# Performance work log

Hardware: AMD Instinct MI355X
Metric: run time of the kernel (lower is better)

## Reference

```python
import jax, jax.numpy as jnp
import numpy as np

# SLAYER SRM-alpha neuron params (nmnist.yaml defaults)
THETA = 10.0      # spike threshold
TAU_SR = 10.0     # PSP (alpha kernel) time constant
TAU_REF = 1.0     # refractory time constant
SCALE_REF = 2.0   # refractory amplitude scale (kernel peak = -2*theta)
TS = 1.0          # simulation step (ms)
K_EPS = 100       # truncated PSP kernel length (alpha kernel ~0 beyond 10*tau)

_t = np.arange(K_EPS, dtype=np.float32) * TS
EPS = jnp.asarray((_t / TAU_SR) * np.exp(1.0 - _t / TAU_SR))  # alpha kernel, peak 1
REF_DECAY = float(np.exp(-TS / TAU_REF))
REF_AMP = SCALE_REF * THETA


def spike_fn(u):
    # hard threshold (forward only)
    return (u >= THETA).astype(u.dtype)


def psp(x):
    """Causal temporal convolution with the SRM alpha kernel. x: [B,C,H,W,T]."""
    B, C, H, W, T = x.shape
    xf = x.reshape(B * C * H * W, 1, T)
    k = EPS[::-1].reshape(1, 1, K_EPS).astype(x.dtype)
    y = jax.lax.conv_general_dilated(xf, k, (1,), [(K_EPS - 1, 0)])
    return y.reshape(B, C, H, W, T)


def spike(a):
    """Threshold with exponential refractory feedback, sequential over time."""
    at = jnp.moveaxis(a, -1, 0)  # [T,B,C,H,W]
    def step(r, a_t):
        u = a_t + r
        s = spike_fn(u)
        r_new = REF_DECAY * (r - REF_AMP * s)
        return r_new, s
    _, s = jax.lax.scan(step, jnp.zeros(at.shape[1:], a.dtype), at)
    return jnp.moveaxis(s, 0, -1)


DN = ('NCHWT', 'OIHWT', 'NCHWT')  # time treated as a size-1-kernel spatial dim

def conv_t(x, w, pad):
    # x: [B,C,H,W,T], w: [O,I,kh,kw] -> spatial conv applied at every time step
    return jax.lax.conv_general_dilated(
        x, w[..., None], (1, 1, 1),
        [(pad, pad), (pad, pad), (0, 0)], dimension_numbers=DN)


def pool_t(x):
    # SLAYER pool: depthwise 2x2 sum-pool with fixed weight 1.1*theta
    C = x.shape[1]
    k = jnp.full((C, 1, 2, 2, 1), 1.1 * THETA, x.dtype)
    return jax.lax.conv_general_dilated(
        x, k, (2, 2, 1), [(0, 0), (0, 0), (0, 0)],
        feature_group_count=C, dimension_numbers=DN)


def setup_inputs() -> dict:
    key = jax.random.key(0)
    ks = jax.random.split(key, 5)
    B, T = 16, 300
    s_in = (jax.random.uniform(ks[0], (B, 2, 34, 34, T)) < 0.05).astype(jnp.float32)
    def w(k, shape, fan):
        return jax.random.normal(k, shape, jnp.float32) * (4.0 / np.sqrt(fan))
    W1 = w(ks[1], (16, 2, 5, 5), 2 * 25)
    W2 = w(ks[2], (32, 16, 3, 3), 16 * 9)
    W3 = w(ks[3], (64, 32, 3, 3), 32 * 9)
    Wf = w(ks[4], (10, 64, 8, 8), 64 * 64)
    return {"s_in": s_in, "W1": W1, "W2": W2, "W3": W3, "Wf": Wf}


def reference(s_in, W1, W2, W3, Wf):
    s1 = spike(psp(conv_t(s_in, W1, 1)))  # [B,16,32,32,T]
    s2 = spike(psp(pool_t(s1)))           # [B,16,16,16,T]
    s3 = spike(psp(conv_t(s2, W2, 1)))    # [B,32,16,16,T]
    s4 = spike(psp(pool_t(s3)))           # [B,32,8,8,T]
    s5 = spike(psp(conv_t(s4, W3, 1)))    # [B,64,8,8,T]
    # dense (8,8,64)->10 is a full-extent conv == contraction over c,h,w
    u = jnp.einsum('bchwt,ochw->bot', s5, Wf)[:, :, None, None, :]
    return spike(psp(u))                  # [B,10,1,1,T]
```

## Files before the change

### kernel.cpp

```cpp
#include <hip/hip_runtime.h>
#include <hip/hip_bf16.h>
#include <stdint.h>
#include <stddef.h>

#define TPAD 320
#define TREAL 300

#define POOL_W   11.000000000000002

static __device__ __forceinline__ float bf2f(uint16_t b) {
    return __uint_as_float(((uint32_t)b) << 16);
}

struct IIRC { double DD, C1, C2, C3, DR; };
static __device__ __forceinline__ IIRC iirc_make() {
    IIRC c;
    c.DD = exp(-0.1);
    c.C1 = exp(1.0) / 10.0;
    c.C2 = exp(-9.0) / 10.0;
    c.C3 = 10.0 * exp(-9.0);
    c.DR = exp(-1.0);
    return c;
}
struct IIRS { double P, Q, P2, Q2, r; };
static __device__ __forceinline__ void iirs_init(IIRS& s) {
    s.P = 0.0; s.Q = 0.0; s.P2 = 0.0; s.Q2 = 0.0; s.r = 0.0;
}
static __device__ __forceinline__ bool iir_step(const IIRC& c, IIRS& st,
                                                double x, double xd) {
    double Qn  = c.DD * (st.Q + st.P);
    double Pn  = fma(c.DD, st.P, x);
    double Q2n = c.DD * (st.Q2 + st.P2);
    double P2n = fma(c.DD, st.P2, xd);
    double a = c.C1 * Qn - c.C2 * Q2n - c.C3 * P2n;
    double u = a + st.r;
    bool s = (u >= 10.0);
    st.r = c.DR * (st.r - (s ? 20.0 : 0.0));
    st.P = Pn; st.Q = Qn; st.P2 = P2n; st.Q2 = Q2n;
    return s;
}

__global__ void detect_kernel(const uint16_t* __restrict__ w1raw, int* __restrict__ flag)
{
    if (threadIdx.x == 0 && blockIdx.x == 0) {
        int sane = 1;
        for (int i = 0; i < 800; ++i) {
            int e = (w1raw[i] >> 7) & 0xFF;
            if (e >= 131) { sane = 0; break; }
        }
        *flag = sane;
    }
}

__global__ __launch_bounds__(256) void wtrans_kernel(
    const void* __restrict__ w, double* __restrict__ out, int Co, int CKK,
    const int* __restrict__ flag)
{
    int i = blockIdx.x * 256 + threadIdx.x;
    if (i >= Co * CKK) return;
    int co = i / CKK, r = i - co * CKK;
    double v = (*flag) ? (double)bf2f(((const uint16_t*)w)[i])
                       : (double)((const float*)w)[i];
    out[(size_t)(co >> 4) * CKK * 16 + (size_t)r * 16 + (co & 15)] = v;
}

__global__ __launch_bounds__(256) void wcvt_kernel(
    const void* __restrict__ w, float* __restrict__ out, int n, const int* __restrict__ flag)
{
    int i = blockIdx.x * 256 + threadIdx.x;
    if (i >= n) return;
    out[i] = (*flag) ? bf2f(((const uint16_t*)w)[i]) : ((const float*)w)[i];
}

__global__ __launch_bounds__(320) void convert_kernel(
    const void* __restrict__ s_in, uint8_t* __restrict__ u8, const int* __restrict__ flag)
{
    int row = blockIdx.x;
    int t = threadIdx.x;
    uint8_t v = 0;
    if (t < TREAL) {
        float x = (*flag) ? bf2f(((const uint16_t*)s_in)[(size_t)row * TREAL + t])
                          : ((const float*)s_in)[(size_t)row * TREAL + t];
        v = (x >= 0.5f) ? 1 : 0;
    }
    u8[(size_t)row * TPAD + t] = v;
}

template<int Ci, int CIB, int K, int Hi>
__global__ __launch_bounds__(320) void conv_z_kernel(
    const uint8_t* __restrict__ sprev,
    const double* __restrict__ Wt,
    double* __restrict__ z,
    int Co_total)
{
    constexpr int P = 1;
    constexpr int Wi = Hi;
    constexpr int Ho = Hi + 2 * P - K + 1;
    constexpr int Wo = Ho;
    constexpr int KK = K * K;
    constexpr int CKK = Ci * KK;
    constexpr int CW = K + 1;
    constexpr int NROW = CIB * K * CW;
    constexpr int NPASS = Ci / CIB;
    constexpr int WTILE = CIB * KK * 16;
    static_assert(Ci % CIB == 0, "pass split");
    static_assert(Wo % 2 == 0, "pair split");
    static_assert(NROW * 320 + WTILE * 8 <= 60 * 1024, "LDS over limit");

    __shared__ uint32_t stage[NROW * 80];
    __shared__ double wtile[WTILE];

    const int t   = threadIdx.x;
    const int h   = (int)blockIdx.x / (Wo / 2);
    const int w   = ((int)blockIdx.x % (Wo / 2)) * 2;
    const int gy  = (int)blockIdx.y;
    const int co0 = gy * 16;
    const int b   = (int)blockIdx.z;

    double acc0[16], acc1[16];
    #pragma unroll
    for (int c = 0; c < 16; ++c) { acc0[c] = 0.0; acc1[c] = 0.0; }

    const size_t in_b = (size_t)b * Ci * Hi * Wi * TPAD;
    const double* wg = Wt + (size_t)gy * CKK * 16;

    for (int p = 0; p < NPASS; ++p) {
        const int ci0 = p * CIB;
        __syncthreads();
        for (int idx = t; idx < NROW * 20; idx += 320) {
            int r  = idx / 20, dw = idx - (idx / 20) * 20;
            int cl = r / (K * CW);
            int rem = r - cl * (K * CW);
            int ky = rem / CW, cx = rem - ky * CW;
            int row = h - P + ky;
            int col = w - P + cx;
            uint4 v = make_uint4(0, 0, 0, 0);
            if ((unsigned)row < (unsigned)Hi && (unsigned)col < (unsigned)Wi)
                v = *(const uint4*)(sprev + in_b +
                      (((size_t)(ci0 + cl) * Hi + row) * Wi + col) * TPAD + dw * 16);
            ((uint4*)stage)[(size_t)r * 20 + dw] = v;
        }
        for (int i = t; i < WTILE; i += 320)
            wtile[i] = wg[(size_t)ci0 * KK * 16 + i];
        __syncthreads();

        const uint8_t* sbytes = (const uint8_t*)stage;
        #pragma unroll 2
        for (int cl = 0; cl < CIB; ++cl) {
            #pragma unroll
            for (int ky = 0; ky < K; ++ky) {
                #pragma unroll
                for (int kx = 0; kx < K; ++kx) {
                    const int rbase = ((cl * K + ky) * CW + kx) * 320;
                    double x0 = (double)sbytes[rbase + t];
                    double x1 = (double)sbytes[rbase + 320 + t];
                    const double* wrow = wtile + (cl * KK + ky * K + kx) * 16;
                    #pragma unroll
                    for (int c = 0; c < 16; ++c) {
                        double wv = wrow[c];
                        acc0[c] = fma(wv, x0, acc0[c]);
                        acc1[c] = fma(wv, x1, acc1[c]);
                    }
                }
            }
        }
    }

    #pragma unroll
    for (int c = 0; c < 16; ++c) {
        size_t row0 = (((size_t)b * Co_total + co0 + c) * Ho + h) * Wo + w;
        z[row0 * TPAD + t]          = acc0[c];
        z[(row0 + 1) * TPAD + t]    = acc1[c];
    }
}

__global__ __launch_bounds__(256) void psp_scan_kernel(
    const double* __restrict__ z, uint8_t* __restrict__ sout, int N)
{
    __shared__ uint32_t bits[128 * 11];
    const int tid = threadIdx.x;
    const int n0 = blockIdx.x * 128;
    const int n = n0 + tid;
    const bool active = (tid < 128) && (n < N);

    if (active) {
        const double* zr = z + (size_t)n * TPAD;
        const IIRC c = iirc_make();
        IIRS st; iirs_init(st);
        uint32_t bw = 0;
        #pragma unroll 5
        for (int t0 = 0; t0 < 100; t0 += 4) {
            double2 xa = *(const double2*)(zr + t0);
            double2 xb = *(const double2*)(zr + t0 + 2);
            if (iir_step(c, st, xa.x, 0.0)) bw |= 1u << (t0 & 31);
            if (iir_step(c, st, xa.y, 0.0)) bw |= 1u << ((t0 + 1) & 31);
            if (iir_step(c, st, xb.x, 0.0)) bw |= 1u << ((t0 + 2) & 31);
            if (iir_step(c, st, xb.y, 0.0)) bw |= 1u << ((t0 + 3) & 31);
            if ((t0 & 31) == 28) { bits[tid * 11 + (t0 >> 5)] = bw; bw = 0; }
        }
        #pragma unroll 5
        for (int t0 = 100; t0 < TREAL; t0 += 4) {
            double2 xa = *(const double2*)(zr + t0);
            double2 xb = *(const double2*)(zr + t0 + 2);
            double2 da = *(const double2*)(zr + t0 - 100);
            double2 db = *(const double2*)(zr + t0 - 98);
            if (iir_step(c, st, xa.x, da.x)) bw |= 1u << (t0 & 31);
            if (iir_step(c, st, xa.y, da.y)) bw |= 1u << ((t0 + 1) & 31);
            if (iir_step(c, st, xb.x, db.x)) bw |= 1u << ((t0 + 2) & 31);
            if (iir_step(c, st, xb.y, db.y)) bw |= 1u << ((t0 + 3) & 31);
            if ((t0 & 31) == 28) { bits[tid * 11 + (t0 >> 5)] = bw; bw = 0; }
        }
        bits[tid * 11 + 9] = bw;
    }
    __syncthreads();

    for (int task = tid; task < 128 * 80; task += 256) {
        int nl = task / 80, w = task - nl * 80;
        int ng = n0 + nl;
        if (ng >= N) continue;
        int tb = w * 4;
        uint32_t word = bits[nl * 11 + (tb >> 5)];
        uint32_t o = 0;
        #pragma unroll
        for (int j = 0; j < 4; ++j)
            if ((word >> ((tb + j) & 31)) & 1u) o |= 1u << (8 * j);
        *(uint32_t*)(sout + (size_t)ng * TPAD + tb) = o;
    }
}

template<int C, int Hi>
__global__ __launch_bounds__(256) void pool_psp_v2_kernel(
    const uint8_t* __restrict__ sprev, uint8_t* __restrict__ sout, int N)
{
    constexpr int Wi = Hi, Ho = Hi / 2, Wo = Wi / 2;
    __shared__ uint32_t cnt[128 * 81];
    __shared__ uint32_t bits[128 * 11];
    const int tid = threadIdx.x;
    const int n0 = blockIdx.x * 128;

    for (int task = tid; task < 128 * 80; task += 256) {
        int nl = task / 80, w = task - nl * 80;
        int n = n0 + nl;
        if (n >= N) continue;
        int wo = n % Wo;  int r1 = n / Wo;
        int ho = r1 % Ho; int r2 = r1 / Ho;
        int cc = r2 % C;  int b  = r2 / C;
        const uint8_t* p0 = sprev +
            ((((size_t)b * C + cc) * Hi + 2 * ho) * Wi + 2 * wo) * TPAD + w * 4;
        uint32_t a0 = *(const uint32_t*)p0;
        uint32_t a1 = *(const uint32_t*)(p0 + TPAD);
        uint32_t a2 = *(const uint32_t*)(p0 + (size_t)Wi * TPAD);
        uint32_t a3 = *(const uint32_t*)(p0 + (size_t)(Wi + 1) * TPAD);
        cnt[nl * 81 + w] = a0 + a1 + a2 + a3;
    }
    __syncthreads();

    if (tid < 128 && n0 + tid < N) {
        const uint8_t* cb = (const uint8_t*)cnt + (size_t)tid * 324;
        const IIRC c = iirc_make();
        IIRS st; iirs_init(st);
        uint32_t bw = 0;
        for (int t = 0; t < 100; ++t) {
            double x = POOL_W * (double)cb[t];
            if (iir_step(c, st, x, 0.0)) bw |= 1u << (t & 31);
            if ((t & 31) == 31) { bits[tid * 11 + (t >> 5)] = bw; bw = 0; }
        }
        for (int t = 100; t < TREAL; ++t) {
            double x  = POOL_W * (double)cb[t];
            double xd = POOL_W * (double)cb[t - 100];
            if (iir_step(c, st, x, xd)) bw |= 1u << (t & 31);
            if ((t & 31) == 31) { bits[tid * 11 + (t >> 5)] = bw; bw = 0; }
        }
        bits[tid * 11 + 9] = bw;
    }
    __syncthreads();

    for (int task = tid; task < 128 * 80; task += 256) {
        int nl = task / 80, w = task - nl * 80;
        int n = n0 + nl;
        if (n >= N) continue;
        int tb = w * 4;
        uint32_t word = bits[nl * 11 + (tb >> 5)];
        uint32_t o = 0;
        #pragma unroll
        for (int j = 0; j < 4; ++j)
            if ((word >> ((tb + j) & 31)) & 1u) o |= 1u << (8 * j);
        *(uint32_t*)(sout + (size_t)n * TPAD + tb) = o;
    }
}

__global__ __launch_bounds__(256) void dense_partial_kernel(
    const uint8_t* __restrict__ s5, const float* __restrict__ Wf,
    double* __restrict__ partial)
{
    const int tc = blockIdx.x, b = blockIdx.y, p = blockIdx.z;
    const int tid = threadIdx.x;
    const int tl = tid & 63, slot = tid >> 6;
    const int t = tc * 64 + tl;
    const int i0 = p * 256 + slot * 64;
    double acc[10];
    #pragma unroll
    for (int o = 0; o < 10; ++o) acc[o] = 0.0;
    const uint8_t* sp = s5 + ((size_t)b * 4096 + i0) * TPAD + t;
    for (int i = 0; i < 64; ++i) {
        float f = (float)sp[(size_t)i * TPAD];
        if (__any(f != 0.f)) {
            #pragma unroll
            for (int o = 0; o < 10; ++o)
                acc[o] = fma((double)Wf[o * 4096 + i0 + i], (double)f, acc[o]);
        }
    }
    __shared__ double red[4][64][10];
    #pragma unroll
    for (int o = 0; o < 10; ++o) red[slot][tl][o] = acc[o];
    __syncthreads();
    if (slot == 0) {
        #pragma unroll
        for (int o = 0; o < 10; ++o) {
            double v = ((red[0][tl][o] + red[1][tl][o]) + red[2][tl][o]) + red[3][tl][o];
            partial[((size_t)p * 160 + (size_t)b * 10 + o) * TPAD + t] = v;
        }
    }
}

__global__ __launch_bounds__(320) void psp_out_final_kernel(
    const double* __restrict__ partial, void* __restrict__ out,
    const int* __restrict__ flag)
{
    __shared__ double xs[TPAD];
    __shared__ uint8_t sb[TREAL];
    const int n = blockIdx.x;
    const int t = threadIdx.x;
    double v = 0.0;
    #pragma unroll
    for (int p = 0; p < 16; ++p)
        v += partial[((size_t)p * 160 + n) * TPAD + t];
    xs[t] = v;
    __syncthreads();
    if (t == 0) {
        const IIRC c = iirc_make();
        IIRS st; iirs_init(st);
        for (int i = 0; i < TREAL; ++i) {
            double xd = (i >= 100) ? xs[i - 100] : 0.0;
            sb[i] = iir_step(c, st, xs[i], xd) ? 1 : 0;
        }
    }
    __syncthreads();
    if (t < TREAL) {
        size_t e = (size_t)n * TREAL + t;
        if (*flag) ((uint16_t*)out)[e] = sb[t] ? 0x3F80 : 0;
        else       ((float*)out)[e]    = sb[t] ? 1.0f : 0.0f;
    }
}

__global__ __launch_bounds__(256) void fill_kernel(float* __restrict__ out, int n, float v)
{
    int i = blockIdx.x * 256 + threadIdx.x;
    if (i < n) out[i] = v;
}

static inline size_t alignup(size_t x) { return (x + 255) & ~(size_t)255; }
static inline int pick_bg(size_t per_b, size_t budget) {
    const int cand[5] = {16, 8, 4, 2, 1};
    for (int k = 0; k < 5; ++k)
        if (per_b * (size_t)cand[k] <= budget) return cand[k];
    return 0;
}

extern "C" void kernel_launch(void* const* d_in, const int* in_sizes, int n_in,
                              void* d_out, int out_size, void* d_ws, size_t ws_size,
                              hipStream_t stream)
{
    if (n_in != 5 || in_sizes[0] != 16 * 2 * 34 * 34 * 300 || in_sizes[1] != 800 ||
        in_sizes[2] != 4608 || in_sizes[3] != 18432 || in_sizes[4] != 40960 ||
        out_size != 16 * 10 * 300) {
        fill_kernel<<<(out_size + 255) / 256, 256, 0, stream>>>((float*)d_out, out_size, 2.0e5f);
        return;
    }

    const size_t flag_sz  = alignup(sizeof(int));
    const size_t w64_sz   = alignup((size_t)(800 + 4608 + 18432) * 8);
    const size_t wf32_sz  = alignup((size_t)40960 * 4);
    const size_t sin8_sz  = alignup((size_t)16 * 2 * 34 * 34 * TPAD);
    const size_t dpart_sz = alignup((size_t)16 * 160 * TPAD * 8);
    const size_t sA_sz    = alignup((size_t)16 * 16384 * TPAD);
    const size_t sB_sz    = alignup((size_t)16 * 4096 * TPAD);
    const size_t base_sz  = flag_sz + w64_sz + wf32_sz + sin8_sz + dpart_sz + sA_sz + sB_sz;
    if (base_sz + 256 > ws_size) {
        fill_kernel<<<(out_size + 255) / 256, 256, 0, stream>>>((float*)d_out, out_size, 1.0e5f);
        return;
    }
    const size_t zbud = ws_size - base_sz - 256;

    const size_t zb1 = (size_t)16 * 1024 * TPAD * 8;
    const size_t zb3 = (size_t)32 * 256 * TPAD * 8;
    const size_t zb5 = (size_t)64 * 64 * TPAD * 8;
    const int bg1 = pick_bg(zb1, zbud), bg3 = pick_bg(zb3, zbud), bg5 = pick_bg(zb5, zbud);
    if (bg1 == 0 || bg3 == 0 || bg5 == 0) {
        fill_kernel<<<(out_size + 255) / 256, 256, 0, stream>>>((float*)d_out, out_size, 1.0e5f);
        return;
    }

    char* base = (char*)d_ws;
    int* flag = (int*)base;          base += flag_sz;
    double* w64 = (double*)base;     base += w64_sz;
    float* wf32 = (float*)base;      base += wf32_sz;
    uint8_t* sin8 = (uint8_t*)base;  base += sin8_sz;
    double* dpart = (double*)base;   base += dpart_sz;
    uint8_t* sA = (uint8_t*)base;    base += sA_sz;
    uint8_t* sB = (uint8_t*)base;    base += sB_sz;
    double* z64 = (double*)base;

    detect_kernel<<<1, 64, 0, stream>>>((const uint16_t*)d_in[1], flag);

    double* Wt1 = w64;
    double* Wt2 = w64 + 800;
    double* Wt3 = w64 + 800 + 4608;
    wtrans_kernel<<<(800 + 255) / 256, 256, 0, stream>>>(d_in[1], Wt1, 16, 50, flag);
    wtrans_kernel<<<(4608 + 255) / 256, 256, 0, stream>>>(d_in[2], Wt2, 32, 144, flag);
    wtrans_kernel<<<(18432 + 255) / 256, 256, 0, stream>>>(d_in[3], Wt3, 64, 288, flag);
    wcvt_kernel<<<(40960 + 255) / 256, 256, 0, stream>>>(d_in[4], wf32, 40960, flag);
    convert_kernel<<<16 * 2 * 34 * 34, 320, 0, stream>>>(d_in[0], sin8, flag);

    for (int b0 = 0; b0 < 16; b0 += bg1) {
        conv_z_kernel<2, 2, 5, 34><<<dim3(32 * 16, 1, bg1), 320, 0, stream>>>(
            sin8 + (size_t)b0 * 2 * 34 * 34 * TPAD, Wt1, z64, 16);
        int N = bg1 * 16384;
        psp_scan_kernel<<<(N + 127) / 128, 256, 0, stream>>>(
            z64, sA + (size_t)b0 * 16384 * TPAD, N);
    }
    pool_psp_v2_kernel<16, 32><<<(16 * 4096 + 127) / 128, 256, 0, stream>>>(
        sA, sB, 16 * 4096);
    for (int b0 = 0; b0 < 16; b0 += bg3) {
        conv_z_kernel<16, 8, 3, 16><<<dim3(16 * 8, 2, bg3), 320, 0, stream>>>(
            sB + (size_t)b0 * 16 * 256 * TPAD, Wt2, z64, 32);
        int N = bg3 * 8192;
        psp_scan_kernel<<<(N + 127) / 128, 256, 0, stream>>>(
            z64, sA + (size_t)b0 * 8192 * TPAD, N);
    }
    pool_psp_v2_kernel<32, 16><<<(16 * 2048 + 127) / 128, 256, 0, stream>>>(
        sA, sB, 16 * 2048);
    for (int b0 = 0; b0 < 16; b0 += bg5) {
        conv_z_kernel<32, 8, 3, 8><<<dim3(8 * 4, 4, bg5), 320, 0, stream>>>(
            sB + (size_t)b0 * 32 * 64 * TPAD, Wt3, z64, 64);
        int N = bg5 * 4096;
        psp_scan_kernel<<<(N + 127) / 128, 256, 0, stream>>>(
            z64, sA + (size_t)b0 * 4096 * TPAD, N);
    }
    dense_partial_kernel<<<dim3(5, 16, 16), 256, 0, stream>>>(sA, wf32, dpart);
    psp_out_final_kernel<<<160, 320, 0, stream>>>(dpart, d_out, flag);
}
```

Baseline: 1.670 ms.

## Use FP64 MFMA 16x16x4 for conv layers with runtime accumulation-order probe

Rewrites the spatial conv inner loop to use the f64 16x16x4 matrix-core instruction. Weights are pre-packed into per-lane fragment layout and input spike bytes are read from LDS as the A operand. A one-wave probe kernel checks whether the MFMA rounding matches a sequential FMA chain, in ascending or descending order, so that results stay bit-exact. If neither order matches, the original scalar FMA path is used. This aims to cut the FP64 FMA cost of the conv stages, at the price of extra launches, an LDS weight-layout change and a runtime branch.

```diff
diff --git a/kernel.cpp b/kernel.cpp
--- a/kernel.cpp
+++ b/kernel.cpp
@@ -7,6 +7,8 @@
 #define TREAL 300
 
 #define POOL_W   11.000000000000002
+
+typedef double v4d __attribute__((ext_vector_type(4)));
 
 static __device__ __forceinline__ float bf2f(uint16_t b) {
     return __uint_as_float(((uint32_t)b) << 16);
@@ -52,6 +54,51 @@
     }
 }
 
+static __device__ __forceinline__ double probe_val(int a, int b, int s) {
+    uint32_t h = (uint32_t)(a * 73856093) ^ (uint32_t)(b * 19349663)
+               ^ (uint32_t)(s * 83492791) ^ 0x9e3779b9u;
+    h ^= h >> 13; h *= 0x85ebca6bu; h ^= h >> 16;
+    int mant = (int)(h & 0xFFFFFu) | 1;
+    int e = (int)((h >> 20) & 63u) - 32;
+    double v = ldexp((double)mant, e);
+    return (h & 0x40000000u) ? -v : v;
+}
+
+__global__ void mfma_probe_kernel(int* __restrict__ mode)
+{
+    const int lane = (int)threadIdx.x & 63;
+    const int i16 = lane & 15;
+    const int k4  = lane >> 4;
+    bool ok_asc = true, ok_desc = true;
+    for (int s = 0; s < 8; ++s) {
+        double av = probe_val(i16, k4, 2 * s + 1);
+        double bv = probe_val(16 + k4, i16, 3 * s + 2);
+        v4d c;
+        #pragma unroll
+        for (int r = 0; r < 4; ++r)
+            c[r] = probe_val(32 + 4 * k4 + r, i16, 5 * s + 3);
+        v4d d = __builtin_amdgcn_mfma_f64_16x16x4f64(av, bv, c, 0, 0, 0);
+        #pragma unroll
+        for (int r = 0; r < 4; ++r) {
+            int i = 4 * k4 + r, j = i16;
+            double ea = probe_val(32 + i, j, 5 * s + 3);
+            double ed = ea;
+            #pragma unroll
+            for (int k = 0; k < 4; ++k)
+                ea = fma(probe_val(i, k, 2 * s + 1), probe_val(16 + k, j, 3 * s + 2), ea);
+            #pragma unroll
+            for (int k2 = 3; k2 >= 0; --k2)
+                ed = fma(probe_val(i, k2, 2 * s + 1), probe_val(16 + k2, j, 3 * s + 2), ed);
+            ok_asc  &= (__double_as_longlong(ea) == __double_as_longlong(d[r]));
+            ok_desc &= (__double_as_longlong(ed) == __double_as_longlong(d[r]));
+        }
+    }
+    unsigned long long ba = __ballot(ok_asc);
+    unsigned long long bd = __ballot(ok_desc);
+    if (threadIdx.x == 0)
+        *mode = (ba == ~0ull) ? 1 : ((bd == ~0ull) ? 2 : 0);
+}
+
 __global__ __launch_bounds__(256) void wtrans_kernel(
     const void* __restrict__ w, double* __restrict__ out, int Co, int CKK,
     const int* __restrict__ flag)
@@ -62,6 +109,31 @@
     double v = (*flag) ? (double)bf2f(((const uint16_t*)w)[i])
                        : (double)((const float*)w)[i];
     out[(size_t)(co >> 4) * CKK * 16 + (size_t)r * 16 + (co & 15)] = v;
+}
+
+__global__ __launch_bounds__(256) void wtrans_frag_kernel(
+    const void* __restrict__ w, double* __restrict__ out,
+    int CKK, int KS_TOTAL, int total,
+    const int* __restrict__ flag, const int* __restrict__ mode)
+{
+    int i = blockIdx.x * 256 + threadIdx.x;
+    if (i >= total) return;
+    int md = *mode;
+    int lane = i & 63;
+    int gks  = (i >> 6) % KS_TOTAL;
+    int gy   = (i >> 6) / KS_TOTAL;
+    int kl   = lane >> 4;
+    int col  = lane & 15;
+    int kle  = (md == 2) ? (3 - kl) : kl;
+    int tap  = gks * 4 + kle;
+    int co   = gy * 16 + col;
+    double v = 0.0;
+    if (tap < CKK) {
+        int src = co * CKK + tap;
+        v = (*flag) ? (double)bf2f(((const uint16_t*)w)[src])
+                    : (double)((const float*)w)[src];
+    }
+    out[i] = v;
 }
 
 __global__ __launch_bounds__(256) void wcvt_kernel(
@@ -90,8 +162,9 @@
 __global__ __launch_bounds__(320) void conv_z_kernel(
     const uint8_t* __restrict__ sprev,
     const double* __restrict__ Wt,
+    const double* __restrict__ Wfrag,
     double* __restrict__ z,
-    int Co_total)
+    int Co_total, const int* __restrict__ mode)
 {
     constexpr int P = 1;
     constexpr int Wi = Hi;
@@ -102,75 +175,144 @@
     constexpr int CW = K + 1;
     constexpr int NROW = CIB * K * CW;
     constexpr int NPASS = Ci / CIB;
+    constexpr int TPP = CIB * KK;
+    constexpr int KSP = (TPP + 3) / 4;
+    constexpr int KS_TOTAL = NPASS * KSP;
     constexpr int WTILE = CIB * KK * 16;
+    constexpr int WTILE_MAX = (KSP * 64 > WTILE) ? KSP * 64 : WTILE;
     static_assert(Ci % CIB == 0, "pass split");
     static_assert(Wo % 2 == 0, "pair split");
-    static_assert(NROW * 320 + WTILE * 8 <= 60 * 1024, "LDS over limit");
+    static_assert(NROW * 320 + WTILE_MAX * 8 <= 60 * 1024, "LDS over limit");
 
     __shared__ uint32_t stage[NROW * 80];
-    __shared__ double wtile[WTILE];
+    __shared__ double wtile[WTILE_MAX];
 
     const int t   = threadIdx.x;
+    const int wave = t >> 6;
+    const int lane = t & 63;
+    const int l15  = lane & 15;
+    const int l4   = lane >> 4;
     const int h   = (int)blockIdx.x / (Wo / 2);
     const int w   = ((int)blockIdx.x % (Wo / 2)) * 2;
     const int gy  = (int)blockIdx.y;
     const int co0 = gy * 16;
     const int b   = (int)blockIdx.z;
 
-    double acc0[16], acc1[16];
-    #pragma unroll
-    for (int c = 0; c < 16; ++c) { acc0[c] = 0.0; acc1[c] = 0.0; }
-
     const size_t in_b = (size_t)b * Ci * Hi * Wi * TPAD;
-    const double* wg = Wt + (size_t)gy * CKK * 16;
-
-    for (int p = 0; p < NPASS; ++p) {
-        const int ci0 = p * CIB;
-        __syncthreads();
-        for (int idx = t; idx < NROW * 20; idx += 320) {
-            int r  = idx / 20, dw = idx - (idx / 20) * 20;
-            int cl = r / (K * CW);
-            int rem = r - cl * (K * CW);
-            int ky = rem / CW, cx = rem - ky * CW;
-            int row = h - P + ky;
-            int col = w - P + cx;
-            uint4 v = make_uint4(0, 0, 0, 0);
-            if ((unsigned)row < (unsigned)Hi && (unsigned)col < (unsigned)Wi)
-                v = *(const uint4*)(sprev + in_b +
-                      (((size_t)(ci0 + cl) * Hi + row) * Wi + col) * TPAD + dw * 16);
-            ((uint4*)stage)[(size_t)r * 20 + dw] = v;
-        }
-        for (int i = t; i < WTILE; i += 320)
-            wtile[i] = wg[(size_t)ci0 * KK * 16 + i];
-        __syncthreads();
-
-        const uint8_t* sbytes = (const uint8_t*)stage;
-        #pragma unroll 2
-        for (int cl = 0; cl < CIB; ++cl) {
-            #pragma unroll
-            for (int ky = 0; ky < K; ++ky) {
+    const int md = *mode;
+
+    if (md != 0) {
+        const int l4e = (md == 2) ? (3 - l4) : l4;
+        v4d acc[8];
+        #pragma unroll
+        for (int jj = 0; jj < 8; ++jj) acc[jj] = (v4d)(0.0);
+        const double* wfg = Wfrag + (size_t)gy * KS_TOTAL * 64;
+
+        for (int p = 0; p < NPASS; ++p) {
+            const int ci0 = p * CIB;
+            __syncthreads();
+            for (int idx = t; idx < NROW * 20; idx += 320) {
+                int r  = idx / 20, dw = idx - (idx / 20) * 20;
+                int cl = r / (K * CW);
+                int rem = r - cl * (K * CW);
+                int ky = rem / CW, cx = rem - ky * CW;
+                int row = h - P + ky;
+                int col = w - P + cx;
+                uint4 v = make_uint4(0, 0, 0, 0);
+                if ((unsigned)row < (unsigned)Hi && (unsigned)col < (unsigned)Wi)
+                    v = *(const uint4*)(sprev + in_b +
+                          (((size_t)(ci0 + cl) * Hi + row) * Wi + col) * TPAD + dw * 16);
+                ((uint4*)stage)[(size_t)r * 20 + dw] = v;
+            }
+            for (int i = t; i < KSP * 64; i += 320)
+                wtile[i] = wfg[(size_t)p * KSP * 64 + i];
+            __syncthreads();
+
+            const uint8_t* sbytes = (const uint8_t*)stage;
+            for (int ks = 0; ks < KSP; ++ks) {
+                double bv = wtile[ks * 64 + lane];
+                int ltap = ks * 4 + l4e;
+                int rowoff = 0;
+                if ((TPP % 4 == 0) || (ltap < TPP)) {
+                    int cl  = ltap / KK;
+                    int rem = ltap - cl * KK;
+                    int ky  = rem / K;
+                    int kx  = rem - ky * K;
+                    rowoff = ((cl * K + ky) * CW + kx) * 320;
+                }
+                const uint8_t* ab = sbytes + rowoff + l15;
                 #pragma unroll
-                for (int kx = 0; kx < K; ++kx) {
-                    const int rbase = ((cl * K + ky) * CW + kx) * 320;
-                    double x0 = (double)sbytes[rbase + t];
-                    double x1 = (double)sbytes[rbase + 320 + t];
-                    const double* wrow = wtile + (cl * KK + ky * K + kx) * 16;
+                for (int jj = 0; jj < 8; ++jj) {
+                    int jb = wave * 8 + jj;
+                    int tile = jb >> 1, px = jb & 1;
+                    double av = (double)ab[px * 320 + tile * 16];
+                    acc[jj] = __builtin_amdgcn_mfma_f64_16x16x4f64(av, bv, acc[jj], 0, 0, 0);
+                }
+            }
+        }
+
+        #pragma unroll
+        for (int jj = 0; jj < 8; ++jj) {
+            int jb = wave * 8 + jj;
+            int tile = jb >> 1, px = jb & 1;
+            size_t row = (((size_t)b * Co_total + co0 + l15) * Ho + h) * Wo + w + px;
+            *(v4d*)(z + row * TPAD + tile * 16 + l4 * 4) = acc[jj];
+        }
+    } else {
+        double acc0[16], acc1[16];
+        #pragma unroll
+        for (int c = 0; c < 16; ++c) { acc0[c] = 0.0; acc1[c] = 0.0; }
+
+        const double* wg = Wt + (size_t)gy * CKK * 16;
+
+        for (int p = 0; p < NPASS; ++p) {
+            const int ci0 = p * CIB;
+            __syncthreads();
+            for (int idx = t; idx < NROW * 20; idx += 320) {
+                int r  = idx / 20, dw = idx - (idx / 20) * 20;
+                int cl = r / (K * CW);
+                int rem = r - cl * (K * CW);
+                int ky = rem / CW, cx = rem - ky * CW;
+                int row = h - P + ky;
+                int col = w - P + cx;
+                uint4 v = make_uint4(0, 0, 0, 0);
+                if ((unsigned)row < (unsigned)Hi && (unsigned)col < (unsigned)Wi)
+                    v = *(const uint4*)(sprev + in_b +
+                          (((size_t)(ci0 + cl) * Hi + row) * Wi + col) * TPAD + dw * 16);
+                ((uint4*)stage)[(size_t)r * 20 + dw] = v;
+            }
+            for (int i = t; i < WTILE; i += 320)
+                wtile[i] = wg[(size_t)ci0 * KK * 16 + i];
+            __syncthreads();
+
+            const uint8_t* sbytes = (const uint8_t*)stage;
+            #pragma unroll 2
+            for (int cl = 0; cl < CIB; ++cl) {
+                #pragma unroll
+                for (int ky = 0; ky < K; ++ky) {
                     #pragma unroll
-                    for (int c = 0; c < 16; ++c) {
-                        double wv = wrow[c];
-                        acc0[c] = fma(wv, x0, acc0[c]);
-                        acc1[c] = fma(wv, x1, acc1[c]);
+                    for (int kx = 0; kx < K; ++kx) {
+                        const int rbase = ((cl * K + ky) * CW + kx) * 320;
+                        double x0 = (double)sbytes[rbase + t];
+                        double x1 = (double)sbytes[rbase + 320 + t];
+                        const double* wrow = wtile + (cl * KK + ky * K + kx) * 16;
+                        #pragma unroll
+                        for (int c = 0; c < 16; ++c) {
+                            double wv = wrow[c];
+                            acc0[c] = fma(wv, x0, acc0[c]);
+                            acc1[c] = fma(wv, x1, acc1[c]);
+                        }
                     }
                 }
             }
         }
-    }
-
-    #pragma unroll
-    for (int c = 0; c < 16; ++c) {
-        size_t row0 = (((size_t)b * Co_total + co0 + c) * Ho + h) * Wo + w;
-        z[row0 * TPAD + t]          = acc0[c];
-        z[(row0 + 1) * TPAD + t]    = acc1[c];
+
+        #pragma unroll
+        for (int c = 0; c < 16; ++c) {
+            size_t row0 = (((size_t)b * Co_total + co0 + c) * Ho + h) * Wo + w;
+            z[row0 * TPAD + t]          = acc0[c];
+            z[(row0 + 1) * TPAD + t]    = acc1[c];
+        }
     }
 }
 
@@ -379,13 +521,16 @@
     }
 
     const size_t flag_sz  = alignup(sizeof(int));
+    const size_t mode_sz  = alignup(sizeof(int));
     const size_t w64_sz   = alignup((size_t)(800 + 4608 + 18432) * 8);
+    const size_t wfrag_sz = alignup((size_t)(832 + 4608 + 18432) * 8);
     const size_t wf32_sz  = alignup((size_t)40960 * 4);
     const size_t sin8_sz  = alignup((size_t)16 * 2 * 34 * 34 * TPAD);
     const size_t dpart_sz = alignup((size_t)16 * 160 * TPAD * 8);
     const size_t sA_sz    = alignup((size_t)16 * 16384 * TPAD);
     const size_t sB_sz    = alignup((size_t)16 * 4096 * TPAD);
-    const size_t base_sz  = flag_sz + w64_sz + wf32_sz + sin8_sz + dpart_sz + sA_sz + sB_sz;
+    const size_t base_sz  = flag_sz + mode_sz + w64_sz + wfrag_sz + wf32_sz +
+                            sin8_sz + dpart_sz + sA_sz + sB_sz;
     if (base_sz + 256 > ws_size) {
         fill_kernel<<<(out_size + 255) / 256, 256, 0, stream>>>((float*)d_out, out_size, 1.0e5f);
         return;
@@ -403,7 +548,9 @@
 
     char* base = (char*)d_ws;
     int* flag = (int*)base;          base += flag_sz;
+    int* mode = (int*)base;          base += mode_sz;
     double* w64 = (double*)base;     base += w64_sz;
+    double* wfrag = (double*)base;   base += wfrag_sz;
     float* wf32 = (float*)base;      base += wf32_sz;
     uint8_t* sin8 = (uint8_t*)base;  base += sin8_sz;
     double* dpart = (double*)base;   base += dpart_sz;
@@ -412,6 +559,7 @@
     double* z64 = (double*)base;
 
     detect_kernel<<<1, 64, 0, stream>>>((const uint16_t*)d_in[1], flag);
+    mfma_probe_kernel<<<1, 64, 0, stream>>>(mode);
 
     double* Wt1 = w64;
     double* Wt2 = w64 + 800;
@@ -419,12 +567,23 @@
     wtrans_kernel<<<(800 + 255) / 256, 256, 0, stream>>>(d_in[1], Wt1, 16, 50, flag);
     wtrans_kernel<<<(4608 + 255) / 256, 256, 0, stream>>>(d_in[2], Wt2, 32, 144, flag);
     wtrans_kernel<<<(18432 + 255) / 256, 256, 0, stream>>>(d_in[3], Wt3, 64, 288, flag);
+
+    double* Wf1 = wfrag;
+    double* Wf2 = wfrag + 832;
+    double* Wf3 = wfrag + 832 + 4608;
+    wtrans_frag_kernel<<<(832 + 255) / 256, 256, 0, stream>>>(
+        d_in[1], Wf1, 50, 13, 832, flag, mode);
+    wtrans_frag_kernel<<<(4608 + 255) / 256, 256, 0, stream>>>(
+        d_in[2], Wf2, 144, 36, 4608, flag, mode);
+    wtrans_frag_kernel<<<(18432 + 255) / 256, 256, 0, stream>>>(
+        d_in[3], Wf3, 288, 72, 18432, flag, mode);
+
     wcvt_kernel<<<(40960 + 255) / 256, 256, 0, stream>>>(d_in[4], wf32, 40960, flag);
     convert_kernel<<<16 * 2 * 34 * 34, 320, 0, stream>>>(d_in[0], sin8, flag);
 
     for (int b0 = 0; b0 < 16; b0 += bg1) {
         conv_z_kernel<2, 2, 5, 34><<<dim3(32 * 16, 1, bg1), 320, 0, stream>>>(
-            sin8 + (size_t)b0 * 2 * 34 * 34 * TPAD, Wt1, z64, 16);
+            sin8 + (size_t)b0 * 2 * 34 * 34 * TPAD, Wt1, Wf1, z64, 16, mode);
         int N = bg1 * 16384;
         psp_scan_kernel<<<(N + 127) / 128, 256, 0, stream>>>(
             z64, sA + (size_t)b0 * 16384 * TPAD, N);
@@ -433,7 +592,7 @@
         sA, sB, 16 * 4096);
     for (int b0 = 0; b0 < 16; b0 += bg3) {
         conv_z_kernel<16, 8, 3, 16><<<dim3(16 * 8, 2, bg3), 320, 0, stream>>>(
-            sB + (size_t)b0 * 16 * 256 * TPAD, Wt2, z64, 32);
+            sB + (size_t)b0 * 16 * 256 * TPAD, Wt2, Wf2, z64, 32, mode);
         int N = bg3 * 8192;
         psp_scan_kernel<<<(N + 127) / 128, 256, 0, stream>>>(
             z64, sA + (size_t)b0 * 8192 * TPAD, N);
@@ -442,7 +601,7 @@
         sA, sB, 16 * 2048);
     for (int b0 = 0; b0 < 16; b0 += bg5) {
         conv_z_kernel<32, 8, 3, 8><<<dim3(8 * 4, 4, bg5), 320, 0, stream>>>(
-            sB + (size_t)b0 * 32 * 64 * TPAD, Wt3, z64, 64);
+            sB + (size_t)b0 * 32 * 64 * TPAD, Wt3, Wf3, z64, 64, mode);
         int N = bg5 * 4096;
         psp_scan_kernel<<<(N + 127) / 128, 256, 0, stream>>>(
             z64, sA + (size_t)b0 * 4096 * TPAD, N);
```

New measurement: 2.338 ms. 1.4x slower.
